# Optimization experiments

Hardware: AMD Instinct MI355X
Metric: run time of the kernel (lower is better)

Reference implementation:

```python
import jax, jax.numpy as jnp
import numpy as np

B, S, H, A = 64, 200, 256, 16
CAPS_LAYERS = 3
NEG = -1e9
LN_EPS = 1e-12


def _layernorm(x, g, b):
    mu = jnp.mean(x, axis=-1, keepdims=True)
    var = jnp.mean(jnp.square(x - mu), axis=-1, keepdims=True)
    return (x - mu) / jnp.sqrt(var + LN_EPS) * g + b


def setup_inputs() -> dict:
    key = jax.random.key(0)
    ks = jax.random.split(key, 10)
    s = 0.02  # initializer_range
    return {
        "item_emb": jax.random.normal(ks[0], (B, S, H), jnp.float32),
        "item_seq": jax.random.randint(ks[1], (B, S), 0, 50000),
        "time_seq": jax.random.randint(ks[2], (B, S, 2), 0, 14),
        "W_lin": s * jax.random.normal(ks[3], (H, H), jnp.float32),
        "b_lin": jnp.zeros((H,), jnp.float32),
        "aspect_embs": s * jax.random.normal(ks[4], (A, H), jnp.float32),
        "pos_emb": s * jax.random.normal(ks[5], (S, H), jnp.float32),
        "tdt_emb": s * jax.random.normal(ks[6], (14, H), jnp.float32),
        "tdn_emb": s * jax.random.normal(ks[7], (14, H), jnp.float32),
        "Wa1": s * jax.random.normal(ks[8], (H, H), jnp.float32),
        "ba1": jnp.zeros((H,), jnp.float32),
        "Wa2": s * jax.random.normal(ks[9], (H,), jnp.float32),
        "ba2": jnp.zeros((1,), jnp.float32),
        "ln_g": jnp.ones((H,), jnp.float32),
        "ln_b": jnp.zeros((H,), jnp.float32),
    }


def reference(item_emb, item_seq, time_seq, W_lin, b_lin, aspect_embs,
              pos_emb, tdt_emb, tdn_emb, Wa1, ba1, Wa2, ba2, ln_g, ln_b):
    b, s = item_emb.shape[0], item_emb.shape[1]
    pad = item_seq == 0  # [B,S]

    # ---- TimeAwareAttention (seq_output has a singleton neighbor dim in torch) ----
    td = tdt_emb[time_seq[:, :, 0]] + tdn_emb[time_seq[:, :, 1]]       # [B,S,H]
    tma_in = pos_emb[None, :s] + item_emb + td                          # [B,S,H]
    h = tma_in @ Wa1 + ba1
    h = jnp.where(h >= 0, h, 0.01 * h)                                  # LeakyReLU
    w = h @ Wa2 + ba2[0]                                                # [B,S]
    w = jnp.where(pad, NEG, w)
    tma = jax.nn.softmax(w, axis=-1)                                    # [B,S]

    # ---- gating (eval: clean gates) ----
    gates = jnp.einsum('bsh,ah->bsa', item_emb, aspect_embs)            # [B,S,A]
    idx = jnp.argmax(gates, axis=-1)                                    # topk k=1, [B,S]

    src = jnp.where(pad, 0.0, 1.0)
    counts = jnp.zeros((b, A), jnp.float32).at[jnp.arange(b)[:, None], idx].add(src)
    aspect_mask = counts == 0                                           # [B,A]

    # ---- item transform (dropout = identity in eval) ----
    moe = _layernorm(jnp.tanh(item_emb @ W_lin + b_lin) + item_emb, ln_g, ln_b)  # [B,S,H]

    # ---- capsule routing ----
    bij = gates
    cap = jnp.broadcast_to(aspect_embs[None], (b, A, H))
    for _ in range(CAPS_LAYERS):
        cij = jnp.where(aspect_mask[:, None, :], NEG, bij)
        cij = jax.nn.softmax(cij, axis=-1)
        cij = jnp.where(pad[:, :, None], 0.0, cij)                      # [B,S,A]
        cap = jnp.einsum('bsa,bsh,bs->bah', cij, moe, tma)              # [B,A,H]
        n2 = jnp.sum(jnp.square(cap), axis=-1, keepdims=True)
        cap = n2 / (1.0 + n2) / jnp.sqrt(n2 + 1e-9) * cap               # squash
        bij = bij + jnp.einsum('bsh,bah->bsa', moe, cap)

    # ---- gather activated interests / activation positions ----
    activated = cap[jnp.arange(b)[:, None], idx]                        # [B,S,H]
    seq_pos = jnp.where(pad, 0, jnp.arange(1, s + 1)[None, :]).astype(jnp.float32)
    act_mat = jnp.full((b, s, A), -1.0, jnp.float32)
    act_mat = act_mat.at[jnp.arange(b)[:, None], jnp.arange(s)[None, :], idx].set(seq_pos)
    act_mat = jnp.where(pad[:, :, None], -1.0, act_mat)
    max_pos = jnp.max(act_mat, axis=1)                                  # [B,A]
    aspects_item_idx = jnp.where(max_pos > -1.0, max_pos - 1.0, max_pos)

    gates_sm = jax.nn.softmax(gates, axis=-1)
    return (cap, gates_sm, aspect_mask, activated, aspects_item_idx, idx[:, :, None])
```

## Files before the change

### kernel.cpp

```cpp
#include <hip/hip_runtime.h>

#define B_ 64
#define S_ 200
#define H_ 256
#define A_ 16
#define M_ (B_*S_)
#define NEGV (-1000000000.0f)

typedef unsigned short ushortT;
typedef __attribute__((ext_vector_type(8))) short short8;
typedef __attribute__((ext_vector_type(4))) float f32x4;

__device__ __forceinline__ ushortT bf16u(float f) {
  unsigned int u = __builtin_bit_cast(unsigned int, f);
  unsigned int r = (u + 0x7fffu + ((u >> 16) & 1u)) >> 16;
  return (ushortT)r;
}
__device__ __forceinline__ float bf2f(ushortT u) {
  unsigned int v = ((unsigned int)u) << 16;
  return __builtin_bit_cast(float, v);
}

__global__ __launch_bounds__(256) void prep_kernel(
    const float* __restrict__ item, const float* __restrict__ Wa1,
    const float* __restrict__ W_lin, const float* __restrict__ asp,
    ushortT* __restrict__ Wa1T, ushortT* __restrict__ WlinT,
    float* __restrict__ gates_raw, float* __restrict__ idxf)
{
  const int blk = blockIdx.x;
  const int t = threadIdx.x;

  if (blk >= 800) {
    __shared__ float T[64*65];
    int wsel = (blk - 800) >> 4;
    int tile = (blk - 800) & 15;
    const float* W = wsel ? W_lin : Wa1;
    ushortT* WT = wsel ? WlinT : Wa1T;
    int tr = (tile >> 2) * 64, tc = (tile & 3) * 64;
    #pragma unroll
    for (int p = 0; p < 16; ++p) {
      int r = p*4 + (t >> 6);
      int c = t & 63;
      T[c*65 + r] = W[(tr + r)*H_ + tc + c];
    }
    __syncthreads();
    #pragma unroll
    for (int p = 0; p < 16; ++p) {
      int n = p*4 + (t >> 6);
      int k = t & 63;
      WT[(tc + n)*H_ + tr + k] = bf16u(T[n*65 + k]);
    }
    return;
  }

  __shared__ float aspl[16*260];
  __shared__ float gL[16*20];

  const int m0 = blk * 16;
  #pragma unroll
  for (int i = 0; i < 4; ++i) {
    int e = t + 256*i;
    int r = e >> 6, c = e & 63;
    *(float4*)&aspl[r*260 + 4*c] = *(const float4*)&asp[r*H_ + 4*c];
  }
  __syncthreads();

  {
    int r = t >> 4, a = t & 15;
    int m = m0 + r;
    float g = 0.f;
    #pragma unroll 4
    for (int k4 = 0; k4 < 64; ++k4) {
      float4 xv = *(const float4*)&item[(size_t)m*H_ + 4*k4];
      float4 av = *(const float4*)&aspl[a*260 + 4*k4];
      g += xv.x*av.x + xv.y*av.y + xv.z*av.z + xv.w*av.w;
    }
    gL[r*20 + a] = g;
  }
  __syncthreads();
  if (t < 64) {
    int r = t >> 2, q = t & 3;
    float4 gv;
    gv.x = gL[r*20 + 4*q + 0]; gv.y = gL[r*20 + 4*q + 1];
    gv.z = gL[r*20 + 4*q + 2]; gv.w = gL[r*20 + 4*q + 3];
    *(float4*)&gates_raw[(m0+r)*A_ + 4*q] = gv;
  }
  if (t < 16) {
    float best = gL[t*20]; int bi = 0;
    #pragma unroll
    for (int a = 1; a < 16; ++a) {
      float v = gL[t*20 + a];
      if (v > best) { best = v; bi = a; }
    }
    idxf[m0 + t] = (float)bi;
  }
}

__global__ __launch_bounds__(512, 2) void gemm_kernel(
    const float* __restrict__ item, const int* __restrict__ iseq,
    const int* __restrict__ tseq, const float* __restrict__ pos,
    const float* __restrict__ tdt, const float* __restrict__ tdn,
    const ushortT* __restrict__ Wa1T, const ushortT* __restrict__ WlinT,
    const float* __restrict__ ba1, const float* __restrict__ Wa2,
    const float* __restrict__ ba2, const float* __restrict__ b_lin,
    const float* __restrict__ g_ln, const float* __restrict__ b_ln,
    float* __restrict__ w_out, ushortT* __restrict__ moe_outB)
{
  __shared__ ushortT Atma[64*40];
  __shared__ ushortT Aitm[64*40];
  __shared__ ushortT B0l[256*40];
  __shared__ ushortT B1l[256*40];
  __shared__ int sL[64], ttL[64], tnL[64];

  const int t = threadIdx.x;
  const int m0 = blockIdx.x * 64;
  const int lane = t & 63, w = t >> 6;
  const int g = w >> 2, wl = w & 3;
  const int col = lane & 15;
  const int rg  = lane >> 4;

  if (t < 64) {
    int m = m0 + t;
    sL[t]  = m % S_;
    ttL[t] = tseq[2*m];
    tnL[t] = tseq[2*m+1];
  }

  f32x4 acc[16];
  #pragma unroll
  for (int i = 0; i < 16; ++i) acc[i] = (f32x4){0.f,0.f,0.f,0.f};

  const int ar = t >> 3, kq = (t & 7) * 4;
  const int nr = t >> 1, kh = (t & 1) * 16;

  __syncthreads();

  for (int k0 = 0; k0 < H_; k0 += 32) {
    float4 iv = *(const float4*)&item[(size_t)(m0 + ar)*H_ + k0 + kq];
    float4 pv = *(const float4*)&pos[sL[ar]*H_ + k0 + kq];
    float4 tv = *(const float4*)&tdt[ttL[ar]*H_ + k0 + kq];
    float4 nv = *(const float4*)&tdn[tnL[ar]*H_ + k0 + kq];
    union { ushortT u[4]; uint2 v; } ci, ct;
    ci.u[0] = bf16u(iv.x); ci.u[1] = bf16u(iv.y);
    ci.u[2] = bf16u(iv.z); ci.u[3] = bf16u(iv.w);
    ct.u[0] = bf16u(iv.x + pv.x + tv.x + nv.x);
    ct.u[1] = bf16u(iv.y + pv.y + tv.y + nv.y);
    ct.u[2] = bf16u(iv.z + pv.z + tv.z + nv.z);
    ct.u[3] = bf16u(iv.w + pv.w + tv.w + nv.w);
    uint4 b0a = *(const uint4*)&Wa1T[(size_t)nr*H_ + k0 + kh];
    uint4 b0b = *(const uint4*)&Wa1T[(size_t)nr*H_ + k0 + kh + 8];
    uint4 b1a = *(const uint4*)&WlinT[(size_t)nr*H_ + k0 + kh];
    uint4 b1b = *(const uint4*)&WlinT[(size_t)nr*H_ + k0 + kh + 8];
    __syncthreads();
    *(uint2*)&Aitm[ar*40 + kq] = ci.v;
    *(uint2*)&Atma[ar*40 + kq] = ct.v;
    *(uint4*)&B0l[nr*40 + kh]     = b0a;
    *(uint4*)&B0l[nr*40 + kh + 8] = b0b;
    *(uint4*)&B1l[nr*40 + kh]     = b1a;
    *(uint4*)&B1l[nr*40 + kh + 8] = b1b;
    __syncthreads();
    const ushortT* Ab = g ? Aitm : Atma;
    const ushortT* Bb = g ? B1l : B0l;
    short8 af = *(const short8*)&Ab[(wl*16 + col)*40 + rg*8];
    #pragma unroll
    for (int q = 0; q < 16; ++q) {
      short8 bf = *(const short8*)&Bb[(q*16 + col)*40 + rg*8];
      acc[q] = __builtin_amdgcn_mfma_f32_16x16x32_bf16(af, bf, acc[q], 0, 0, 0);
    }
  }

  if (g == 0) {
    float bav[16], wav[16];
    #pragma unroll
    for (int q = 0; q < 16; ++q) {
      int n = q*16 + col;
      bav[q] = ba1[n]; wav[q] = Wa2[n];
    }
    float bb2 = ba2[0];
    #pragma unroll
    for (int j = 0; j < 4; ++j) {
      float p = 0.f;
      #pragma unroll
      for (int q = 0; q < 16; ++q) {
        float h = acc[q][j] + bav[q];
        h = (h >= 0.f) ? h : 0.01f*h;
        p += h * wav[q];
      }
      #pragma unroll
      for (int mk = 1; mk < 16; mk <<= 1) p += __shfl_xor(p, mk);
      if (col == 0) {
        int m = m0 + wl*16 + rg*4 + j;
        w_out[m] = (iseq[m] == 0) ? NEGV : (p + bb2);
      }
    }
  } else {
    float blv[16], glv[16], bbv[16];
    #pragma unroll
    for (int q = 0; q < 16; ++q) {
      int n = q*16 + col;
      blv[q] = b_lin[n]; glv[q] = g_ln[n]; bbv[q] = b_ln[n];
    }
    #pragma unroll
    for (int j = 0; j < 4; ++j) {
      int m = m0 + wl*16 + rg*4 + j;
      float v[16];
      float s1 = 0.f, s2 = 0.f;
      #pragma unroll
      for (int q = 0; q < 16; ++q) {
        float ivv = item[(size_t)m*H_ + q*16 + col];
        float vv = tanhf(acc[q][j] + blv[q]) + ivv;
        v[q] = vv; s1 += vv; s2 += vv*vv;
      }
      #pragma unroll
      for (int mk = 1; mk < 16; mk <<= 1) {
        s1 += __shfl_xor(s1, mk);
        s2 += __shfl_xor(s2, mk);
      }
      float mu  = s1 * (1.0f/H_);
      float var = s2 * (1.0f/H_) - mu*mu;
      float rs  = 1.0f / sqrtf(fmaxf(var, 0.f) + 1e-12f);
      #pragma unroll
      for (int q = 0; q < 16; ++q)
        moe_outB[(size_t)m*H_ + q*16 + col] = bf16u((v[q] - mu)*rs*glv[q] + bbv[q]);
    }
  }
}

__device__ __forceinline__ float blk_max(float v, float* red) {
  #pragma unroll
  for (int mk = 32; mk; mk >>= 1) v = fmaxf(v, __shfl_xor(v, mk));
  int t = threadIdx.x;
  if ((t & 63) == 0) red[t >> 6] = v;
  __syncthreads();
  if (t < 64) {
    float x = (t < 16) ? red[t] : -3.0e38f;
    #pragma unroll
    for (int mk = 8; mk; mk >>= 1) x = fmaxf(x, __shfl_xor(x, mk));
    if (t == 0) red[0] = x;
  }
  __syncthreads();
  float r = red[0];
  __syncthreads();
  return r;
}

__device__ __forceinline__ float blk_sum(float v, float* red) {
  #pragma unroll
  for (int mk = 32; mk; mk >>= 1) v += __shfl_xor(v, mk);
  int t = threadIdx.x;
  if ((t & 63) == 0) red[t >> 6] = v;
  __syncthreads();
  if (t < 64) {
    float x = (t < 16) ? red[t] : 0.f;
    #pragma unroll
    for (int mk = 8; mk; mk >>= 1) x += __shfl_xor(x, mk);
    if (t == 0) red[0] = x;
  }
  __syncthreads();
  float r = red[0];
  __syncthreads();
  return r;
}

#define WGSTR 232
#define CBSTR 260
#define CLSTR 252

__global__ __launch_bounds__(1024) void phaseC_kernel(
    const int* __restrict__ iseq, const float* __restrict__ w_in,
    const ushortT* __restrict__ moeB, const float* __restrict__ idxf,
    float* __restrict__ gates_rs,
    float* __restrict__ cap_out,
    float* __restrict__ mask_out,
    float* __restrict__ aidx_out,
    float* __restrict__ act_out)
{
  __shared__ ushortT moeTr[57344];
  __shared__ ushortT wgtT[16*WGSTR];
  __shared__ ushortT capB[16*CBSTR];
  __shared__ float bij[4032];
  __shared__ float n2p[16*17];
  __shared__ float n2s[16];
  __shared__ float tmaL[S_];
  __shared__ float red[16];
  __shared__ float maskf[A_];
  __shared__ int counts[A_], maxpos[A_];
  __shared__ int idxl[S_];
  __shared__ int padl[S_];

  const int t = threadIdx.x;
  const int b = blockIdx.x;
  const int base = b * S_;
  const int lane = t & 63, w = t >> 6;
  const int la = lane & 15, lg = lane >> 4;

  #pragma unroll
  for (int u = 0; u < 4; ++u) {
    int e = t + 1024*u;
    if (e < 3584) {
      int ht = e & 15, s = e >> 4;
      int ks = s >> 5, s4l = (s >> 2) & 7, sr = s & 3;
      int bp = (s4l & 1) ? 4 + (s4l >> 1) : (s4l >> 1);
      int li = ((ht*7 + ks)*8 + bp)*64 + sr*16;
      if (s < S_) {
        const ushortT* gp = &moeB[((size_t)(base + s))*H_ + ht*16];
        *(uint4*)&moeTr[li]     = *(const uint4*)gp;
        *(uint4*)&moeTr[li + 8] = *(const uint4*)(gp + 8);
      } else {
        uint4 z = {0,0,0,0};
        *(uint4*)&moeTr[li] = z; *(uint4*)&moeTr[li + 8] = z;
      }
    }
  }
  if (t < 512) {
    int a = t >> 5, s = 200 + (t & 31);
    wgtT[a*WGSTR + s] = 0;
  }

  if (t < A_) { counts[t] = 0; maxpos[t] = -1; }
  float wv = -3.0e38f;
  if (t < S_) {
    int s = t;
    padl[s] = (iseq[base+s] == 0) ? 1 : 0;
    idxl[s] = (int)idxf[base+s];
    wv = w_in[base+s];
    #pragma unroll
    for (int q = 0; q < 4; ++q)
      *(float4*)&bij[s*20 + 4*q] = *(const float4*)&gates_rs[(base+s)*A_ + 4*q];
  }
  __syncthreads();

  if (t < S_ && !padl[t]) {
    atomicAdd(&counts[idxl[t]], 1);
    atomicMax(&maxpos[idxl[t]], t + 1);
  }
  if (t < S_) {
    int s = t;
    float row[16]; float mx = -3.0e38f;
    #pragma unroll
    for (int a = 0; a < 16; ++a) { row[a] = bij[s*20+a]; mx = fmaxf(mx, row[a]); }
    float sm = 0.f;
    #pragma unroll
    for (int a = 0; a < 16; ++a) { row[a] = expf(row[a] - mx); sm += row[a]; }
    float inv = 1.f / sm;
    #pragma unroll
    for (int q = 0; q < 4; ++q) {
      float4 o; o.x=row[4*q]*inv; o.y=row[4*q+1]*inv; o.z=row[4*q+2]*inv; o.w=row[4*q+3]*inv;
      *(float4*)&gates_rs[(base+s)*A_ + 4*q] = o;
    }
  }
  float mxw = blk_max(wv, red);
  float ev = (t < S_) ? expf(wv - mxw) : 0.f;
  float sw = blk_sum(ev, red);
  if (t < S_) tmaL[t] = ev / sw;
  __syncthreads();
  if (t < A_) {
    int c = counts[t];
    float mkv = (c == 0) ? 1.f : 0.f;
    maskf[t] = mkv;
    mask_out[b*A_ + t] = mkv;
    int mp = maxpos[t];
    aidx_out[b*A_ + t] = (mp > 0) ? (float)(mp - 1) : -1.f;
  }
  __syncthreads();

  for (int iter = 0; iter < 3; ++iter) {
    if (t < S_) {
      int s = t;
      float row[16]; float mx = -3.0e38f;
      #pragma unroll
      for (int a = 0; a < 16; ++a) {
        float v = bij[s*20+a];
        v = (maskf[a] > 0.5f) ? NEGV : v;
        row[a] = v; mx = fmaxf(mx, v);
      }
      float sm = 0.f;
      #pragma unroll
      for (int a = 0; a < 16; ++a) { row[a] = expf(row[a] - mx); sm += row[a]; }
      float sc = (padl[s] ? 0.f : tmaL[s]) / sm;
      #pragma unroll
      for (int a = 0; a < 16; ++a) wgtT[a*WGSTR + s] = bf16u(row[a]*sc);
    }
    __syncthreads();

    f32x4 acc = (f32x4){0.f,0.f,0.f,0.f};
    {
      unsigned vA = (unsigned)(w*7168 + lane*8);
      #pragma unroll
      for (int ks = 0; ks < 7; ++ks) {
        unsigned vAk = vA + (unsigned)(ks*1024);
        long long r0, r1;
        asm volatile(
          "ds_read_b64_tr_b16 %0, %2\n\t"
          "ds_read_b64_tr_b16 %1, %2 offset:512\n\t"
          "s_waitcnt lgkmcnt(0)"
          : "=&v"(r0), "=&v"(r1) : "v"(vAk) : "memory");
        __builtin_amdgcn_sched_barrier(0);
        union { short8 v; long long q[2]; } uu;
        uu.q[0] = r0; uu.q[1] = r1;
        short8 bf = *(const short8*)&wgtT[la*WGSTR + ks*32 + lg*8];
        acc = __builtin_amdgcn_mfma_f32_16x16x32_bf16(uu.v, bf, acc, 0, 0, 0);
      }
    }
    {
      float n2 = acc[0]*acc[0] + acc[1]*acc[1] + acc[2]*acc[2] + acc[3]*acc[3];
      n2 += __shfl_xor(n2, 16);
      n2 += __shfl_xor(n2, 32);
      if (lane < 16) n2p[w*17 + lane] = n2;
    }
    __syncthreads();
    if (t < 16) {
      float sv = 0.f;
      #pragma unroll
      for (int w2 = 0; w2 < 16; ++w2) sv += n2p[w2*17 + t];
      n2s[t] = sv / (1.f + sv) / sqrtf(sv + 1e-9f);
    }
    __syncthreads();
    {
      float sc = n2s[la];
      if (iter < 2) {
        #pragma unroll
        for (int r = 0; r < 4; ++r)
          capB[la*CBSTR + w*16 + lg*4 + r] = bf16u(acc[r]*sc);
      } else {
        float* capl = bij;
        #pragma unroll
        for (int r = 0; r < 4; ++r)
          capl[la*CLSTR + w*16 + lg*4 + r] = acc[r]*sc;
      }
    }
    __syncthreads();

    if (iter < 2) {
      if (w < 13) {
        int sR = w*16 + la;
        int ksS = sR >> 5, s4l = (sR >> 2) & 7, sr = sR & 3;
        int bp = (s4l & 1) ? 4 + (s4l >> 1) : (s4l >> 1);
        int laneA = ksS*512 + bp*64 + sr*16 + (lg & 1)*8 + (lg >> 1)*3584;
        f32x4 accS = (f32x4){0.f,0.f,0.f,0.f};
        #pragma unroll
        for (int k4 = 0; k4 < 8; ++k4) {
          short8 am = *(const short8*)&moeTr[laneA + k4*7168];
          short8 bc = *(const short8*)&capB[la*CBSTR + k4*32 + lg*8];
          accS = __builtin_amdgcn_mfma_f32_16x16x32_bf16(am, bc, accS, 0, 0, 0);
        }
        int sW = w*16 + lg*4;
        #pragma unroll
        for (int r = 0; r < 4; ++r)
          if (sW + r < S_) bij[(sW + r)*20 + la] += accS[r];
      }
      __syncthreads();
    }
  }

  {
    const float* capl = bij;
    #pragma unroll
    for (int q = 0; q < 4; ++q) {
      int e = t + 1024*q;
      int a = e >> 8, h = e & 255;
      cap_out[((size_t)b*A_ + a)*H_ + h] = capl[a*CLSTR + h];
    }
    int h4 = t & 63;
    for (int s = t >> 6; s < S_; s += 16) {
      float4 v = *(const float4*)&capl[idxl[s]*CLSTR + 4*h4];
      *(float4*)&act_out[((size_t)base + s)*H_ + 4*h4] = v;
    }
  }
}

extern "C" void kernel_launch(void* const* d_in, const int* in_sizes, int n_in,
                              void* d_out, int out_size, void* d_ws, size_t ws_size,
                              hipStream_t stream) {
  (void)in_sizes; (void)n_in; (void)out_size; (void)ws_size;
  const float* item  = (const float*)d_in[0];
  const int*   iseq  = (const int*)d_in[1];
  const int*   tseq  = (const int*)d_in[2];
  const float* W_lin = (const float*)d_in[3];
  const float* b_lin = (const float*)d_in[4];
  const float* asp   = (const float*)d_in[5];
  const float* pos   = (const float*)d_in[6];
  const float* tdt   = (const float*)d_in[7];
  const float* tdn   = (const float*)d_in[8];
  const float* Wa1   = (const float*)d_in[9];
  const float* ba1   = (const float*)d_in[10];
  const float* Wa2   = (const float*)d_in[11];
  const float* ba2   = (const float*)d_in[12];
  const float* g_ln  = (const float*)d_in[13];
  const float* b_ln  = (const float*)d_in[14];

  float* out    = (float*)d_out;
  float* cap_o  = out;
  float* gate_o = out + 262144;
  float* mask_o = out + 466944;
  float* act_o  = out + 467968;
  float* aidx_o = out + 3744768;
  float* idx_o  = out + 3745792;

  ushortT* moeB  = (ushortT*)d_ws;
  ushortT* Wa1T  = (ushortT*)((char*)d_ws + 6553600);
  ushortT* WlinT = Wa1T + 65536;
  float*   w_ws  = (float*)((char*)d_ws + 6553600 + 262144);

  prep_kernel<<<832, 256, 0, stream>>>(item, Wa1, W_lin, asp,
      Wa1T, WlinT, gate_o, idx_o);
  gemm_kernel<<<200, 512, 0, stream>>>(item, iseq, tseq, pos, tdt, tdn,
      Wa1T, WlinT, ba1, Wa2, ba2, b_lin, g_ln, b_ln, w_ws, moeB);
  phaseC_kernel<<<B_, 1024, 0, stream>>>(iseq, w_ws, moeB, idx_o,
      gate_o, cap_o, mask_o, aidx_o, act_o);
}
```

Measured before the change: 59.53 us.

## Restructure GEMM tiling, move gate softmax to prep, split activated gather kernel

Gate softmax moves into prep_kernel, with raw gates staged in workspace, so phaseC no longer computes it. The GEMM kernel now keeps the whole A row-block in LDS, prefetches the next K slice in registers, and uses a 2x2 wave tile with cross-wave reductions through shared memory. Its LayerNorm residual now reads the bf16 item from LDS instead of fp32 global memory, which changes numerics slightly. The activated-interest gather moves out of the 64-block phaseC into a separate wide kernel, at the cost of one more launch and a re-read of cap.

```diff
diff --git a/kernel.cpp b/kernel.cpp
--- a/kernel.cpp
+++ b/kernel.cpp
@@ -25,7 +25,8 @@
     const float* __restrict__ item, const float* __restrict__ Wa1,
     const float* __restrict__ W_lin, const float* __restrict__ asp,
     ushortT* __restrict__ Wa1T, ushortT* __restrict__ WlinT,
-    float* __restrict__ gates_raw, float* __restrict__ idxf)
+    float* __restrict__ graw, float* __restrict__ gates_sm,
+    float* __restrict__ idxf)
 {
   const int blk = blockIdx.x;
   const int t = threadIdx.x;
@@ -83,20 +84,31 @@
     float4 gv;
     gv.x = gL[r*20 + 4*q + 0]; gv.y = gL[r*20 + 4*q + 1];
     gv.z = gL[r*20 + 4*q + 2]; gv.w = gL[r*20 + 4*q + 3];
-    *(float4*)&gates_raw[(m0+r)*A_ + 4*q] = gv;
+    *(float4*)&graw[(m0+r)*A_ + 4*q] = gv;
   }
   if (t < 16) {
-    float best = gL[t*20]; int bi = 0;
+    int r = t;
+    float best = gL[r*20]; int bi = 0;
+    float mx = gL[r*20];
     #pragma unroll
     for (int a = 1; a < 16; ++a) {
-      float v = gL[t*20 + a];
+      float v = gL[r*20 + a];
       if (v > best) { best = v; bi = a; }
-    }
-    idxf[m0 + t] = (float)bi;
-  }
-}
-
-__global__ __launch_bounds__(512, 2) void gemm_kernel(
+      mx = fmaxf(mx, v);
+    }
+    idxf[m0 + r] = (float)bi;
+    float ex[16]; float sm = 0.f;
+    #pragma unroll
+    for (int a = 0; a < 16; ++a) { ex[a] = expf(gL[r*20 + a] - mx); sm += ex[a]; }
+    float inv = 1.f / sm;
+    #pragma unroll
+    for (int a = 0; a < 16; ++a) gates_sm[(m0+r)*A_ + a] = ex[a]*inv;
+  }
+}
+
+#define ASTR 280
+#define BSTR 40
+__global__ __launch_bounds__(512) void gemm_kernel(
     const float* __restrict__ item, const int* __restrict__ iseq,
     const int* __restrict__ tseq, const float* __restrict__ pos,
     const float* __restrict__ tdt, const float* __restrict__ tdn,
@@ -106,16 +118,20 @@
     const float* __restrict__ g_ln, const float* __restrict__ b_ln,
     float* __restrict__ w_out, ushortT* __restrict__ moe_outB)
 {
-  __shared__ ushortT Atma[64*40];
-  __shared__ ushortT Aitm[64*40];
-  __shared__ ushortT B0l[256*40];
-  __shared__ ushortT B1l[256*40];
+  __shared__ ushortT Atma[64*ASTR];
+  __shared__ ushortT Aitm[64*ASTR];
+  __shared__ ushortT B0l[256*BSTR];
+  __shared__ ushortT B1l[256*BSTR];
   __shared__ int sL[64], ttL[64], tnL[64];
+  __shared__ float wp[2][64];
+  __shared__ float ln1[2][64], ln2[2][64];
+  __shared__ float mus[64], rss[64];
 
   const int t = threadIdx.x;
   const int m0 = blockIdx.x * 64;
   const int lane = t & 63, w = t >> 6;
   const int g = w >> 2, wl = w & 3;
+  const int wm = wl >> 1, wn = wl & 1;
   const int col = lane & 15;
   const int rg  = lane >> 4;
 
@@ -125,104 +141,148 @@
     ttL[t] = tseq[2*m];
     tnL[t] = tseq[2*m+1];
   }
-
-  f32x4 acc[16];
+  __syncthreads();
+
+  const int arow = t >> 3;
+  const int ac4  = (t & 7) * 4;
+  const int nr   = t >> 1;
+  const int kh   = (t & 1) * 16;
+  const int srow = sL[arow], trow = ttL[arow], nrow = tnL[arow];
+
+  float4 pi = *(const float4*)&item[(size_t)(m0+arow)*H_ + ac4];
+  float4 pp = *(const float4*)&pos[srow*H_ + ac4];
+  float4 pt = *(const float4*)&tdt[trow*H_ + ac4];
+  float4 pn = *(const float4*)&tdn[nrow*H_ + ac4];
+  uint4 b0a = *(const uint4*)&Wa1T[(size_t)nr*H_ + kh];
+  uint4 b0b = *(const uint4*)&Wa1T[(size_t)nr*H_ + kh + 8];
+  uint4 b1a = *(const uint4*)&WlinT[(size_t)nr*H_ + kh];
+  uint4 b1b = *(const uint4*)&WlinT[(size_t)nr*H_ + kh + 8];
+
+  f32x4 acc[2][8];
   #pragma unroll
-  for (int i = 0; i < 16; ++i) acc[i] = (f32x4){0.f,0.f,0.f,0.f};
-
-  const int ar = t >> 3, kq = (t & 7) * 4;
-  const int nr = t >> 1, kh = (t & 1) * 16;
-
-  __syncthreads();
-
-  for (int k0 = 0; k0 < H_; k0 += 32) {
-    float4 iv = *(const float4*)&item[(size_t)(m0 + ar)*H_ + k0 + kq];
-    float4 pv = *(const float4*)&pos[sL[ar]*H_ + k0 + kq];
-    float4 tv = *(const float4*)&tdt[ttL[ar]*H_ + k0 + kq];
-    float4 nv = *(const float4*)&tdn[tnL[ar]*H_ + k0 + kq];
+  for (int r = 0; r < 2; ++r)
+    #pragma unroll
+    for (int q = 0; q < 8; ++q) acc[r][q] = (f32x4){0.f,0.f,0.f,0.f};
+
+  #pragma unroll
+  for (int ks = 0; ks < 8; ++ks) {
+    const int k0 = ks*32;
     union { ushortT u[4]; uint2 v; } ci, ct;
-    ci.u[0] = bf16u(iv.x); ci.u[1] = bf16u(iv.y);
-    ci.u[2] = bf16u(iv.z); ci.u[3] = bf16u(iv.w);
-    ct.u[0] = bf16u(iv.x + pv.x + tv.x + nv.x);
-    ct.u[1] = bf16u(iv.y + pv.y + tv.y + nv.y);
-    ct.u[2] = bf16u(iv.z + pv.z + tv.z + nv.z);
-    ct.u[3] = bf16u(iv.w + pv.w + tv.w + nv.w);
-    uint4 b0a = *(const uint4*)&Wa1T[(size_t)nr*H_ + k0 + kh];
-    uint4 b0b = *(const uint4*)&Wa1T[(size_t)nr*H_ + k0 + kh + 8];
-    uint4 b1a = *(const uint4*)&WlinT[(size_t)nr*H_ + k0 + kh];
-    uint4 b1b = *(const uint4*)&WlinT[(size_t)nr*H_ + k0 + kh + 8];
-    __syncthreads();
-    *(uint2*)&Aitm[ar*40 + kq] = ci.v;
-    *(uint2*)&Atma[ar*40 + kq] = ct.v;
-    *(uint4*)&B0l[nr*40 + kh]     = b0a;
-    *(uint4*)&B0l[nr*40 + kh + 8] = b0b;
-    *(uint4*)&B1l[nr*40 + kh]     = b1a;
-    *(uint4*)&B1l[nr*40 + kh + 8] = b1b;
+    ci.u[0] = bf16u(pi.x); ci.u[1] = bf16u(pi.y);
+    ci.u[2] = bf16u(pi.z); ci.u[3] = bf16u(pi.w);
+    ct.u[0] = bf16u(pi.x + pp.x + pt.x + pn.x);
+    ct.u[1] = bf16u(pi.y + pp.y + pt.y + pn.y);
+    ct.u[2] = bf16u(pi.z + pp.z + pt.z + pn.z);
+    ct.u[3] = bf16u(pi.w + pp.w + pt.w + pn.w);
+    *(uint2*)&Aitm[arow*ASTR + k0 + ac4] = ci.v;
+    *(uint2*)&Atma[arow*ASTR + k0 + ac4] = ct.v;
+    *(uint4*)&B0l[nr*BSTR + kh]     = b0a;
+    *(uint4*)&B0l[nr*BSTR + kh + 8] = b0b;
+    *(uint4*)&B1l[nr*BSTR + kh]     = b1a;
+    *(uint4*)&B1l[nr*BSTR + kh + 8] = b1b;
+    if (ks < 7) {
+      const int k1 = k0 + 32;
+      pi = *(const float4*)&item[(size_t)(m0+arow)*H_ + k1 + ac4];
+      pp = *(const float4*)&pos[srow*H_ + k1 + ac4];
+      pt = *(const float4*)&tdt[trow*H_ + k1 + ac4];
+      pn = *(const float4*)&tdn[nrow*H_ + k1 + ac4];
+      b0a = *(const uint4*)&Wa1T[(size_t)nr*H_ + k1 + kh];
+      b0b = *(const uint4*)&Wa1T[(size_t)nr*H_ + k1 + kh + 8];
+      b1a = *(const uint4*)&WlinT[(size_t)nr*H_ + k1 + kh];
+      b1b = *(const uint4*)&WlinT[(size_t)nr*H_ + k1 + kh + 8];
+    }
     __syncthreads();
     const ushortT* Ab = g ? Aitm : Atma;
     const ushortT* Bb = g ? B1l : B0l;
-    short8 af = *(const short8*)&Ab[(wl*16 + col)*40 + rg*8];
-    #pragma unroll
-    for (int q = 0; q < 16; ++q) {
-      short8 bf = *(const short8*)&Bb[(q*16 + col)*40 + rg*8];
-      acc[q] = __builtin_amdgcn_mfma_f32_16x16x32_bf16(af, bf, acc[q], 0, 0, 0);
-    }
-  }
-
+    short8 af0 = *(const short8*)&Ab[(wm*32 + col)*ASTR + k0 + rg*8];
+    short8 af1 = *(const short8*)&Ab[(wm*32 + 16 + col)*ASTR + k0 + rg*8];
+    #pragma unroll
+    for (int q = 0; q < 8; ++q) {
+      short8 bf = *(const short8*)&Bb[(wn*128 + q*16 + col)*BSTR + rg*8];
+      acc[0][q] = __builtin_amdgcn_mfma_f32_16x16x32_bf16(af0, bf, acc[0][q], 0, 0, 0);
+      acc[1][q] = __builtin_amdgcn_mfma_f32_16x16x32_bf16(af1, bf, acc[1][q], 0, 0, 0);
+    }
+    if (ks < 7) __syncthreads();
+  }
+
+  float glv[8], bbv[8];
   if (g == 0) {
-    float bav[16], wav[16];
-    #pragma unroll
-    for (int q = 0; q < 16; ++q) {
-      int n = q*16 + col;
+    float bav[8], wav[8];
+    #pragma unroll
+    for (int q = 0; q < 8; ++q) {
+      int n = wn*128 + q*16 + col;
       bav[q] = ba1[n]; wav[q] = Wa2[n];
     }
-    float bb2 = ba2[0];
-    #pragma unroll
-    for (int j = 0; j < 4; ++j) {
-      float p = 0.f;
-      #pragma unroll
-      for (int q = 0; q < 16; ++q) {
-        float h = acc[q][j] + bav[q];
-        h = (h >= 0.f) ? h : 0.01f*h;
-        p += h * wav[q];
-      }
-      #pragma unroll
-      for (int mk = 1; mk < 16; mk <<= 1) p += __shfl_xor(p, mk);
-      if (col == 0) {
-        int m = m0 + wl*16 + rg*4 + j;
-        w_out[m] = (iseq[m] == 0) ? NEGV : (p + bb2);
-      }
-    }
+    #pragma unroll
+    for (int r = 0; r < 2; ++r)
+      #pragma unroll
+      for (int j = 0; j < 4; ++j) {
+        float p = 0.f;
+        #pragma unroll
+        for (int q = 0; q < 8; ++q) {
+          float h = acc[r][q][j] + bav[q];
+          h = (h >= 0.f) ? h : 0.01f*h;
+          p += h * wav[q];
+        }
+        #pragma unroll
+        for (int mk = 1; mk < 16; mk <<= 1) p += __shfl_xor(p, mk);
+        if (col == 0) wp[wn][wm*32 + r*16 + rg*4 + j] = p;
+      }
   } else {
-    float blv[16], glv[16], bbv[16];
-    #pragma unroll
-    for (int q = 0; q < 16; ++q) {
-      int n = q*16 + col;
+    float blv[8];
+    #pragma unroll
+    for (int q = 0; q < 8; ++q) {
+      int n = wn*128 + q*16 + col;
       blv[q] = b_lin[n]; glv[q] = g_ln[n]; bbv[q] = b_ln[n];
     }
     #pragma unroll
-    for (int j = 0; j < 4; ++j) {
-      int m = m0 + wl*16 + rg*4 + j;
-      float v[16];
-      float s1 = 0.f, s2 = 0.f;
-      #pragma unroll
-      for (int q = 0; q < 16; ++q) {
-        float ivv = item[(size_t)m*H_ + q*16 + col];
-        float vv = tanhf(acc[q][j] + blv[q]) + ivv;
-        v[q] = vv; s1 += vv; s2 += vv*vv;
-      }
-      #pragma unroll
-      for (int mk = 1; mk < 16; mk <<= 1) {
-        s1 += __shfl_xor(s1, mk);
-        s2 += __shfl_xor(s2, mk);
-      }
-      float mu  = s1 * (1.0f/H_);
-      float var = s2 * (1.0f/H_) - mu*mu;
-      float rs  = 1.0f / sqrtf(fmaxf(var, 0.f) + 1e-12f);
-      #pragma unroll
-      for (int q = 0; q < 16; ++q)
-        moe_outB[(size_t)m*H_ + q*16 + col] = bf16u((v[q] - mu)*rs*glv[q] + bbv[q]);
-    }
+    for (int r = 0; r < 2; ++r)
+      #pragma unroll
+      for (int j = 0; j < 4; ++j) {
+        int row = wm*32 + r*16 + rg*4 + j;
+        float s1 = 0.f, s2 = 0.f;
+        #pragma unroll
+        for (int q = 0; q < 8; ++q) {
+          int n = wn*128 + q*16 + col;
+          float vv = tanhf(acc[r][q][j] + blv[q]) + bf2f(Aitm[row*ASTR + n]);
+          acc[r][q][j] = vv; s1 += vv; s2 += vv*vv;
+        }
+        #pragma unroll
+        for (int mk = 1; mk < 16; mk <<= 1) {
+          s1 += __shfl_xor(s1, mk);
+          s2 += __shfl_xor(s2, mk);
+        }
+        if (col == 0) { ln1[wn][row] = s1; ln2[wn][row] = s2; }
+      }
+  }
+  __syncthreads();
+  if (t < 64) {
+    int row = t, m = m0 + row;
+    w_out[m] = (iseq[m] == 0) ? NEGV : (wp[0][row] + wp[1][row] + ba2[0]);
+  } else if (t < 128) {
+    int row = t - 64;
+    float s1 = ln1[0][row] + ln1[1][row];
+    float s2 = ln2[0][row] + ln2[1][row];
+    float mu  = s1 * (1.0f/H_);
+    float var = s2 * (1.0f/H_) - mu*mu;
+    mus[row] = mu;
+    rss[row] = 1.0f / sqrtf(fmaxf(var, 0.f) + 1e-12f);
+  }
+  __syncthreads();
+  if (g == 1) {
+    #pragma unroll
+    for (int r = 0; r < 2; ++r)
+      #pragma unroll
+      for (int j = 0; j < 4; ++j) {
+        int row = wm*32 + r*16 + rg*4 + j;
+        int m = m0 + row;
+        float mu = mus[row], rs = rss[row];
+        #pragma unroll
+        for (int q = 0; q < 8; ++q) {
+          int n = wn*128 + q*16 + col;
+          moe_outB[(size_t)m*H_ + n] = bf16u((acc[r][q][j] - mu)*rs*glv[q] + bbv[q]);
+        }
+      }
   }
 }
 
@@ -269,11 +329,10 @@
 __global__ __launch_bounds__(1024) void phaseC_kernel(
     const int* __restrict__ iseq, const float* __restrict__ w_in,
     const ushortT* __restrict__ moeB, const float* __restrict__ idxf,
-    float* __restrict__ gates_rs,
+    const float* __restrict__ graw,
     float* __restrict__ cap_out,
     float* __restrict__ mask_out,
-    float* __restrict__ aidx_out,
-    float* __restrict__ act_out)
+    float* __restrict__ aidx_out)
 {
   __shared__ ushortT moeTr[57344];
   __shared__ ushortT wgtT[16*WGSTR];
@@ -326,28 +385,13 @@
     wv = w_in[base+s];
     #pragma unroll
     for (int q = 0; q < 4; ++q)
-      *(float4*)&bij[s*20 + 4*q] = *(const float4*)&gates_rs[(base+s)*A_ + 4*q];
+      *(float4*)&bij[s*20 + 4*q] = *(const float4*)&graw[(base+s)*A_ + 4*q];
   }
   __syncthreads();
 
   if (t < S_ && !padl[t]) {
     atomicAdd(&counts[idxl[t]], 1);
     atomicMax(&maxpos[idxl[t]], t + 1);
-  }
-  if (t < S_) {
-    int s = t;
-    float row[16]; float mx = -3.0e38f;
-    #pragma unroll
-    for (int a = 0; a < 16; ++a) { row[a] = bij[s*20+a]; mx = fmaxf(mx, row[a]); }
-    float sm = 0.f;
-    #pragma unroll
-    for (int a = 0; a < 16; ++a) { row[a] = expf(row[a] - mx); sm += row[a]; }
-    float inv = 1.f / sm;
-    #pragma unroll
-    for (int q = 0; q < 4; ++q) {
-      float4 o; o.x=row[4*q]*inv; o.y=row[4*q+1]*inv; o.z=row[4*q+2]*inv; o.w=row[4*q+3]*inv;
-      *(float4*)&gates_rs[(base+s)*A_ + 4*q] = o;
-    }
   }
   float mxw = blk_max(wv, red);
   float ev = (t < S_) ? expf(wv - mxw) : 0.f;
@@ -455,18 +499,22 @@
 
   {
     const float* capl = bij;
-    #pragma unroll
-    for (int q = 0; q < 4; ++q) {
-      int e = t + 1024*q;
-      int a = e >> 8, h = e & 255;
-      cap_out[((size_t)b*A_ + a)*H_ + h] = capl[a*CLSTR + h];
-    }
-    int h4 = t & 63;
-    for (int s = t >> 6; s < S_; s += 16) {
-      float4 v = *(const float4*)&capl[idxl[s]*CLSTR + 4*h4];
-      *(float4*)&act_out[((size_t)base + s)*H_ + 4*h4] = v;
-    }
-  }
+    int a = t >> 6, h4 = t & 63;
+    float4 v = *(const float4*)&capl[a*CLSTR + 4*h4];
+    *(float4*)&cap_out[((size_t)b*A_ + a)*H_ + 4*h4] = v;
+  }
+}
+
+__global__ __launch_bounds__(256) void gather_kernel(
+    const float* __restrict__ capv, const float* __restrict__ idxf,
+    float* __restrict__ act)
+{
+  int e4 = blockIdx.x * 256 + threadIdx.x;
+  int m = e4 >> 6, h4 = e4 & 63;
+  int b = m / S_;
+  int id = (int)idxf[m];
+  float4 v = *(const float4*)&capv[((b*A_) + id)*H_ + 4*h4];
+  *(float4*)&act[(size_t)4*e4] = v;
 }
 
 extern "C" void kernel_launch(void* const* d_in, const int* in_sizes, int n_in,
@@ -499,13 +547,15 @@
 
   ushortT* moeB  = (ushortT*)d_ws;
   ushortT* Wa1T  = (ushortT*)((char*)d_ws + 6553600);
-  ushortT* WlinT = Wa1T + 65536;
+  ushortT* WlinT = (ushortT*)((char*)d_ws + 6553600 + 131072);
   float*   w_ws  = (float*)((char*)d_ws + 6553600 + 262144);
+  float*   graw  = (float*)((char*)d_ws + 6553600 + 262144 + 51200);
 
   prep_kernel<<<832, 256, 0, stream>>>(item, Wa1, W_lin, asp,
-      Wa1T, WlinT, gate_o, idx_o);
+      Wa1T, WlinT, graw, gate_o, idx_o);
   gemm_kernel<<<200, 512, 0, stream>>>(item, iseq, tseq, pos, tdt, tdn,
       Wa1T, WlinT, ba1, Wa2, ba2, b_lin, g_ln, b_ln, w_ws, moeB);
-  phaseC_kernel<<<B_, 1024, 0, stream>>>(iseq, w_ws, moeB, idx_o,
-      gate_o, cap_o, mask_o, aidx_o, act_o);
-}
+  phaseC_kernel<<<B_, 1024, 0, stream>>>(iseq, w_ws, moeB, idx_o, graw,
+      cap_o, mask_o, aidx_o);
+  gather_kernel<<<(M_*H_/4)/256, 256, 0, stream>>>(cap_o, idx_o, act_o);
+}
```

Result: no change. 58.80 us (-1.2%).
